# Performance work log

Measured on AMD Instinct MI355X. Metric: run time of the kernel, lower is better.

## Reference

```python
import jax, jax.numpy as jnp
import numpy as np

N = 50000      # nodes
E = 800000     # edges (avg degree 16)
IN = 128       # in_channels
OUT = 64       # out_channels (latent)
H = 2 * OUT    # hidden = 2*out_channels


def setup_inputs() -> dict:
    key = jax.random.key(0)
    ks = jax.random.split(key, 7)
    s = 0.1
    return {
        "x": jax.random.normal(ks[0], (N, IN), jnp.float32),
        "edge_index": jax.random.randint(ks[1], (2, E), 0, N, dtype=jnp.int64),
        "W1": jax.random.normal(ks[2], (IN, H), jnp.float32) * s,
        "b1": jnp.zeros((H,), jnp.float32),
        "Wmu": jax.random.normal(ks[3], (H, OUT), jnp.float32) * s,
        "bmu": jnp.zeros((OUT,), jnp.float32),
        "Wls": jax.random.normal(ks[4], (H, OUT), jnp.float32) * s,
        "bls": jnp.zeros((OUT,), jnp.float32),
        "eps": jax.random.normal(ks[5], (N, OUT), jnp.float32),
    }


def _gcn_conv(x, W, b, src, dst, dinv):
    # GCNConv: h = W x, out = D^-1/2 (A + I) D^-1/2 h + b
    h = x @ W                                   # [N, F]
    norm = (dinv[src] * dinv[dst])[:, None]     # [E, 1]
    agg = jax.ops.segment_sum(h[src] * norm, dst, num_segments=N)
    agg = agg + h * (dinv * dinv)[:, None]      # self-loop term
    return agg + b


def reference(x, edge_index, W1, b1, Wmu, bmu, Wls, bls, eps):
    src, dst = edge_index[0], edge_index[1]
    # degree with self-loops (PyG gcn_norm counts in-degree on dst/col)
    deg = jax.ops.segment_sum(jnp.ones((E,), x.dtype), dst, num_segments=N) + 1.0
    dinv = deg ** -0.5  # deg >= 1, safe

    h = jax.nn.relu(_gcn_conv(x, W1, b1, src, dst, dinv))
    mu = _gcn_conv(h, Wmu, bmu, src, dst, dinv)
    # Faithful to source bug: logstd also uses convmu weights
    logstd = _gcn_conv(h, Wmu, bmu, src, dst, dinv)
    # training-mode reparameterization with externally supplied noise
    zeta = mu + eps * jnp.exp(logstd)
    return (mu, logstd, zeta)
```

## Files before the change

### kernel.cpp

```cpp
#include <hip/hip_runtime.h>
#include <math.h>

#define N_NODES 50000
#define NPAD    50048
#define N_EDGES 800000
#define IN_C    128
#define H_C     128
#define OUT_C   64
#define BCAP    64
#define EPB     2048

typedef unsigned short u16;
typedef unsigned int   u32;

__device__ __forceinline__ u16 f2bf(float f) {
    u32 u; __builtin_memcpy(&u, &f, 4);
    u += 0x7FFFu + ((u >> 16) & 1u);
    return (u16)(u >> 16);
}
__device__ __forceinline__ float bflo(u32 p) { u32 u = p << 16;         float f; __builtin_memcpy(&f, &u, 4); return f; }
__device__ __forceinline__ float bfhi(u32 p) { u32 u = p & 0xFFFF0000u; float f; __builtin_memcpy(&f, &u, 4); return f; }

__global__ void k_detect_i64(const int* __restrict__ ei, int* __restrict__ flag) {
    int t = threadIdx.x;
    int nz = 0;
    for (int i = t; i < 256; i += 64)
        if (ei[2 * i + 1] != 0) nz = 1;
    unsigned long long b = __ballot(nz != 0);
    if (t == 0) *flag = (b == 0ULL) ? 1 : 0;
}

__device__ __forceinline__ int eidx(const int* __restrict__ ei, size_t pos, int mode) {
    return mode ? ei[pos << 1] : ei[pos];
}

__global__ void k_sort(const int* __restrict__ ei, const int* __restrict__ flag,
                       int* __restrict__ cursor, u16* __restrict__ sorted_src) {
    const int part  = blockIdx.x & 7;
    const int chunk = blockIdx.x >> 3;
    const int base  = chunk * EPB;
    const int m = *flag;
    for (int i = threadIdx.x; i < EPB; i += 256) {
        int e = base + i;
        if (e >= N_EDGES) break;
        int d = eidx(ei, (size_t)N_EDGES + e, m);
        if ((d & 7) != part) continue;
        int s = eidx(ei, (size_t)e, m);
        int c = atomicAdd(&cursor[d], 1);
        if (c < BCAP) sorted_src[((size_t)d << 6) + c] = (u16)s;
    }
}

__global__ void k_dinv(const int* __restrict__ cursor, float* __restrict__ dinv) {
    int i = blockIdx.x * blockDim.x + threadIdx.x;
    if (i < N_NODES) dinv[i] = rsqrtf((float)cursor[i] + 1.0f);
}

__launch_bounds__(256, 4)
__global__ void k_gemm1(const float* __restrict__ X, const float* __restrict__ W,
                        const float* __restrict__ dinv, u16* __restrict__ outq) {
    __shared__ __align__(16) char xs[32768];
    const int tid = threadIdx.x, wv = tid >> 6, lane = tid & 63;
    const int row0 = blockIdx.x * 64 + wv * 16;
    const size_t limit = (size_t)N_NODES * IN_C * 4 - 1024;
    const char* Xb = (const char*)X;

#pragma unroll
    for (int chk = 0; chk < 8; ++chk) {
        size_t off = (size_t)row0 * 512 + (size_t)chk * 1024;
        if (off > limit) off = limit;
        __builtin_amdgcn_global_load_lds(
            (const __attribute__((address_space(1))) void*)(Xb + off + (size_t)lane * 16),
            (__attribute__((address_space(3))) void*)(xs + wv * 8192 + chk * 1024 + lane * 16),
            16, 0, 0);
    }
    asm volatile("s_waitcnt vmcnt(0)" ::: "memory");
    __builtin_amdgcn_sched_barrier(0);

    const int c4 = (lane & 31) * 4;
    const int rs = lane >> 5;

    float4 acc[8];
#pragma unroll
    for (int r = 0; r < 8; ++r) acc[r] = make_float4(0.f, 0.f, 0.f, 0.f);

#pragma unroll 2
    for (int k4 = 0; k4 < IN_C / 4; ++k4) {
        float4 xv[8];
#pragma unroll
        for (int r = 0; r < 8; ++r)
            xv[r] = *reinterpret_cast<const float4*>(
                &xs[wv * 8192 + (rs + r * 2) * 512 + k4 * 16]);
        float4 w0 = *reinterpret_cast<const float4*>(W + (size_t)(4 * k4 + 0) * H_C + c4);
        float4 w1 = *reinterpret_cast<const float4*>(W + (size_t)(4 * k4 + 1) * H_C + c4);
        float4 w2 = *reinterpret_cast<const float4*>(W + (size_t)(4 * k4 + 2) * H_C + c4);
        float4 w3 = *reinterpret_cast<const float4*>(W + (size_t)(4 * k4 + 3) * H_C + c4);
#pragma unroll
        for (int r = 0; r < 8; ++r) {
            acc[r].x = fmaf(xv[r].x, w0.x, acc[r].x);
            acc[r].y = fmaf(xv[r].x, w0.y, acc[r].y);
            acc[r].z = fmaf(xv[r].x, w0.z, acc[r].z);
            acc[r].w = fmaf(xv[r].x, w0.w, acc[r].w);
            acc[r].x = fmaf(xv[r].y, w1.x, acc[r].x);
            acc[r].y = fmaf(xv[r].y, w1.y, acc[r].y);
            acc[r].z = fmaf(xv[r].y, w1.z, acc[r].z);
            acc[r].w = fmaf(xv[r].y, w1.w, acc[r].w);
            acc[r].x = fmaf(xv[r].z, w2.x, acc[r].x);
            acc[r].y = fmaf(xv[r].z, w2.y, acc[r].y);
            acc[r].z = fmaf(xv[r].z, w2.z, acc[r].z);
            acc[r].w = fmaf(xv[r].z, w2.w, acc[r].w);
            acc[r].x = fmaf(xv[r].w, w3.x, acc[r].x);
            acc[r].y = fmaf(xv[r].w, w3.y, acc[r].y);
            acc[r].z = fmaf(xv[r].w, w3.z, acc[r].z);
            acc[r].w = fmaf(xv[r].w, w3.w, acc[r].w);
        }
    }

#pragma unroll
    for (int r = 0; r < 8; ++r) {
        int row = row0 + rs + r * 2;
        if (row < N_NODES) {
            float di = dinv[row];
            ushort4 o;
            o.x = f2bf(acc[r].x * di);
            o.y = f2bf(acc[r].y * di);
            o.z = f2bf(acc[r].z * di);
            o.w = f2bf(acc[r].w * di);
            *reinterpret_cast<ushort4*>(
                outq + (size_t)(c4 >> 4) * (NPAD * 16) + (size_t)row * 16 + (c4 & 15)) = o;
        }
    }
}

__launch_bounds__(256, 4)
__global__ void k_gemm2(const u16* __restrict__ gbuf, const float* __restrict__ W,
                        u16* __restrict__ outp) {
    __shared__ __align__(16) char xs[32768];
    const int tid = threadIdx.x, wv = tid >> 6, lane = tid & 63;
    const int row0 = blockIdx.x * 128 + wv * 32;
    const char* Gb = (const char*)gbuf;

#pragma unroll
    for (int g = 0; g < 8; ++g) {
        size_t off = (size_t)g * (NPAD * 32) + (size_t)row0 * 32;
        __builtin_amdgcn_global_load_lds(
            (const __attribute__((address_space(1))) void*)(Gb + off + (size_t)lane * 16),
            (__attribute__((address_space(3))) void*)(xs + wv * 8192 + g * 1024 + lane * 16),
            16, 0, 0);
    }
    asm volatile("s_waitcnt vmcnt(0)" ::: "memory");
    __builtin_amdgcn_sched_barrier(0);

    const int c4 = (lane & 15) * 4;
    const int rs = lane >> 4;

    float4 acc[8];
#pragma unroll
    for (int r = 0; r < 8; ++r) acc[r] = make_float4(0.f, 0.f, 0.f, 0.f);

#pragma unroll 2
    for (int k4 = 0; k4 < IN_C / 4; ++k4) {
        float4 xv[8];
#pragma unroll
        for (int r = 0; r < 8; ++r) {
            int rl = rs + r * 4;
            uint2 u = *reinterpret_cast<const uint2*>(
                &xs[wv * 8192 + (k4 >> 2) * 1024 + rl * 32 + (k4 & 3) * 8]);
            xv[r].x = bflo(u.x); xv[r].y = bfhi(u.x);
            xv[r].z = bflo(u.y); xv[r].w = bfhi(u.y);
        }
        float4 w0 = *reinterpret_cast<const float4*>(W + (size_t)(4 * k4 + 0) * OUT_C + c4);
        float4 w1 = *reinterpret_cast<const float4*>(W + (size_t)(4 * k4 + 1) * OUT_C + c4);
        float4 w2 = *reinterpret_cast<const float4*>(W + (size_t)(4 * k4 + 2) * OUT_C + c4);
        float4 w3 = *reinterpret_cast<const float4*>(W + (size_t)(4 * k4 + 3) * OUT_C + c4);
#pragma unroll
        for (int r = 0; r < 8; ++r) {
            acc[r].x = fmaf(xv[r].x, w0.x, acc[r].x);
            acc[r].y = fmaf(xv[r].x, w0.y, acc[r].y);
            acc[r].z = fmaf(xv[r].x, w0.z, acc[r].z);
            acc[r].w = fmaf(xv[r].x, w0.w, acc[r].w);
            acc[r].x = fmaf(xv[r].y, w1.x, acc[r].x);
            acc[r].y = fmaf(xv[r].y, w1.y, acc[r].y);
            acc[r].z = fmaf(xv[r].y, w1.z, acc[r].z);
            acc[r].w = fmaf(xv[r].y, w1.w, acc[r].w);
            acc[r].x = fmaf(xv[r].z, w2.x, acc[r].x);
            acc[r].y = fmaf(xv[r].z, w2.y, acc[r].y);
            acc[r].z = fmaf(xv[r].z, w2.z, acc[r].z);
            acc[r].w = fmaf(xv[r].z, w2.w, acc[r].w);
            acc[r].x = fmaf(xv[r].w, w3.x, acc[r].x);
            acc[r].y = fmaf(xv[r].w, w3.y, acc[r].y);
            acc[r].z = fmaf(xv[r].w, w3.z, acc[r].z);
            acc[r].w = fmaf(xv[r].w, w3.w, acc[r].w);
        }
    }

#pragma unroll
    for (int r = 0; r < 8; ++r) {
        int row = row0 + rs + r * 4;
        if (row < N_NODES) {
            ushort4 o;
            o.x = f2bf(acc[r].x);
            o.y = f2bf(acc[r].y);
            o.z = f2bf(acc[r].z);
            o.w = f2bf(acc[r].w);
            *reinterpret_cast<ushort4*>(
                outp + (size_t)(c4 >> 4) * (NPAD * 16) + (size_t)row * 16 + (c4 & 15)) = o;
        }
    }
}

template <int NGRP, int MODE>
__global__ void k_agg(const u16* __restrict__ sorted_src,
                      const int* __restrict__ cursor,
                      const float* __restrict__ dinv,
                      const u16* __restrict__ rows,
                      const float* __restrict__ bias,
                      const float* __restrict__ eps,
                      void* __restrict__ outbuf) {
    const int part  = blockIdx.x & 7;
    const int g     = part % NGRP;
    const int sub   = part / NGRP;
    const int RANGE = N_NODES / (8 / NGRP);
    const int node0 = sub * RANGE + (blockIdx.x >> 3) * 32;
    const int nlim  = sub * RANGE + RANGE;

    const int wv = threadIdx.x >> 6, lane = threadIdx.x & 63;
    const int cl = lane >> 3, pr = lane & 7;
    const int n  = node0 + wv * 8 + cl;
    const bool act = (n < nlim);

    int c = act ? cursor[n] : 0;
    if (c > BCAP) c = BCAP;
    const float di = act ? dinv[n] : 0.f;

    const u32* rw = reinterpret_cast<const u32*>(rows) + (size_t)g * (NPAD * 8);
    const u16* bk = sorted_src + ((size_t)n << 6);

    float a0 = 0.f, a1 = 0.f, b0 = 0.f, b1 = 0.f;
    int j = 0;
    for (; j + 4 <= c; j += 4) {
        ushort4 s4 = *reinterpret_cast<const ushort4*>(bk + j);
        u32 p0 = rw[(size_t)s4.x * 8 + pr];
        u32 p1 = rw[(size_t)s4.y * 8 + pr];
        u32 p2 = rw[(size_t)s4.z * 8 + pr];
        u32 p3 = rw[(size_t)s4.w * 8 + pr];
        a0 += bflo(p0) + bflo(p2);  a1 += bfhi(p0) + bfhi(p2);
        b0 += bflo(p1) + bflo(p3);  b1 += bfhi(p1) + bfhi(p3);
    }
    for (; j < c; ++j) {
        u32 p0 = rw[(size_t)bk[j] * 8 + pr];
        a0 += bflo(p0); a1 += bfhi(p0);
    }
    u32 sn = rw[(size_t)n * 8 + pr];
    const int ch = g * 16 + 2 * pr;
    float s0 = a0 + b0 + bflo(sn);
    float s1 = a1 + b1 + bfhi(sn);

    if (MODE == 0) {
        float px = fmaf(di, s0, bias[ch]);
        float py = fmaf(di, s1, bias[ch + 1]);
        u32 o = (u32)f2bf(di * fmaxf(px, 0.f)) | ((u32)f2bf(di * fmaxf(py, 0.f)) << 16);
        if (act)
            ((u32*)outbuf)[(size_t)g * (NPAD * 8) + (size_t)n * 8 + pr] = o;
    } else if (act) {
        float m0 = fmaf(di, s0, bias[ch]);
        float m1 = fmaf(di, s1, bias[ch + 1]);
        const int NM = N_NODES * OUT_C;
        int i = n * 64 + ch;
        float2 e = *reinterpret_cast<const float2*>(eps + i);
        float z0 = fmaf(e.x, expf(m0), m0);
        float z1 = fmaf(e.y, expf(m1), m1);
        float* o = (float*)outbuf;
        *reinterpret_cast<float2*>(o + i)          = make_float2(m0, m1);
        *reinterpret_cast<float2*>(o + NM + i)     = make_float2(m0, m1);
        *reinterpret_cast<float2*>(o + 2 * NM + i) = make_float2(z0, z1);
    }
}

extern "C" void kernel_launch(void* const* d_in, const int* in_sizes, int n_in,
                              void* d_out, int out_size, void* d_ws, size_t ws_size,
                              hipStream_t stream) {
    const float* x   = (const float*)d_in[0];
    const int*   ei  = (const int*)d_in[1];
    const float* W1  = (const float*)d_in[2];
    const float* b1  = (const float*)d_in[3];
    const float* Wmu = (const float*)d_in[4];
    const float* bmu = (const float*)d_in[5];
    const float* eps = (const float*)d_in[8];
    float* out = (float*)d_out;

    char* p = (char*)d_ws;
    int*  flag   = (int*)p;                        p += 16;
    int*  cursor = (int*)p;                        p += ((size_t)N_NODES * 4 + 15) / 16 * 16;
    float* dinv  = (float*)p;                      p += ((size_t)N_NODES * 4 + 15) / 16 * 16;
    u16* sorted  = (u16*)p;                        p += ((size_t)N_NODES * BCAP * 2 + 15) / 16 * 16;
    u16* bufA    = (u16*)p;                        p += (size_t)8 * NPAD * 32;
    u16* bufG    = (u16*)p;
    u16* bufP    = bufA;

    hipMemsetAsync(cursor, 0, (size_t)N_NODES * sizeof(int), stream);
    k_detect_i64<<<1, 64, 0, stream>>>(ei, flag);
    k_sort<<<8 * ((N_EDGES + EPB - 1) / EPB), 256, 0, stream>>>(ei, flag, cursor, sorted);
    k_dinv<<<(N_NODES + 255) / 256, 256, 0, stream>>>(cursor, dinv);

    k_gemm1<<<(N_NODES + 63) / 64, 256, 0, stream>>>(x, W1, dinv, bufA);
    k_agg<8, 0><<<8 * ((N_NODES + 31) / 32), 256, 0, stream>>>(
        sorted, cursor, dinv, bufA, b1, nullptr, bufG);
    k_gemm2<<<(N_NODES + 127) / 128, 256, 0, stream>>>(bufG, Wmu, bufP);
    k_agg<4, 1><<<8 * ((N_NODES / 2 + 31) / 32), 256, 0, stream>>>(
        sorted, cursor, dinv, bufP, bmu, eps, out);
}
```

Baseline: 202.5 us.

## Widen feature groups to 32 channels and map one wave per node

```diff
diff --git a/kernel.cpp b/kernel.cpp
--- a/kernel.cpp
+++ b/kernel.cpp
@@ -71,7 +71,7 @@
         if (off > limit) off = limit;
         __builtin_amdgcn_global_load_lds(
             (const __attribute__((address_space(1))) void*)(Xb + off + (size_t)lane * 16),
-            (__attribute__((address_space(3))) void*)(xs + wv * 8192 + chk * 1024 + lane * 16),
+            (__attribute__((address_space(3))) void*)(xs + wv * 8192 + chk * 1024),
             16, 0, 0);
     }
     asm volatile("s_waitcnt vmcnt(0)" ::: "memory");
@@ -127,7 +127,7 @@
             o.z = f2bf(acc[r].z * di);
             o.w = f2bf(acc[r].w * di);
             *reinterpret_cast<ushort4*>(
-                outq + (size_t)(c4 >> 4) * (NPAD * 16) + (size_t)row * 16 + (c4 & 15)) = o;
+                outq + (size_t)(c4 >> 5) * (NPAD * 32) + (size_t)row * 32 + (c4 & 31)) = o;
         }
     }
 }
@@ -141,11 +141,12 @@
     const char* Gb = (const char*)gbuf;
 
 #pragma unroll
-    for (int g = 0; g < 8; ++g) {
-        size_t off = (size_t)g * (NPAD * 32) + (size_t)row0 * 32;
+    for (int chk = 0; chk < 8; ++chk) {
+        int g2 = chk >> 1, half = chk & 1;
+        size_t off = (size_t)g2 * (NPAD * 64) + (size_t)(row0 + half * 16) * 64;
         __builtin_amdgcn_global_load_lds(
             (const __attribute__((address_space(1))) void*)(Gb + off + (size_t)lane * 16),
-            (__attribute__((address_space(3))) void*)(xs + wv * 8192 + g * 1024 + lane * 16),
+            (__attribute__((address_space(3))) void*)(xs + wv * 8192 + chk * 1024),
             16, 0, 0);
     }
     asm volatile("s_waitcnt vmcnt(0)" ::: "memory");
@@ -165,7 +166,7 @@
         for (int r = 0; r < 8; ++r) {
             int rl = rs + r * 4;
             uint2 u = *reinterpret_cast<const uint2*>(
-                &xs[wv * 8192 + (k4 >> 2) * 1024 + rl * 32 + (k4 & 3) * 8]);
+                &xs[wv * 8192 + (k4 >> 3) * 2048 + rl * 64 + (k4 & 7) * 8]);
             xv[r].x = bflo(u.x); xv[r].y = bfhi(u.x);
             xv[r].z = bflo(u.y); xv[r].w = bfhi(u.y);
         }
@@ -204,7 +205,7 @@
             o.z = f2bf(acc[r].z);
             o.w = f2bf(acc[r].w);
             *reinterpret_cast<ushort4*>(
-                outp + (size_t)(c4 >> 4) * (NPAD * 16) + (size_t)row * 16 + (c4 & 15)) = o;
+                outp + (size_t)(c4 >> 5) * (NPAD * 32) + (size_t)row * 32 + (c4 & 31)) = o;
         }
     }
 }
@@ -217,63 +218,59 @@
                       const float* __restrict__ bias,
                       const float* __restrict__ eps,
                       void* __restrict__ outbuf) {
-    const int part  = blockIdx.x & 7;
-    const int g     = part % NGRP;
-    const int sub   = part / NGRP;
+    const int part = blockIdx.x & 7;
+    const int g    = part % NGRP;
+    const int sub  = part / NGRP;
     const int RANGE = N_NODES / (8 / NGRP);
-    const int node0 = sub * RANGE + (blockIdx.x >> 3) * 32;
-    const int nlim  = sub * RANGE + RANGE;
 
     const int wv = threadIdx.x >> 6, lane = threadIdx.x & 63;
-    const int cl = lane >> 3, pr = lane & 7;
-    const int n  = node0 + wv * 8 + cl;
-    const bool act = (n < nlim);
-
-    int c = act ? cursor[n] : 0;
-    if (c > BCAP) c = BCAP;
-    const float di = act ? dinv[n] : 0.f;
-
-    const u32* rw = reinterpret_cast<const u32*>(rows) + (size_t)g * (NPAD * 8);
+    const int e4 = lane >> 4, pr = lane & 15;
+    const int n  = sub * RANGE + (blockIdx.x >> 3) * 4 + wv;
+
+    int c = cursor[n]; if (c > BCAP) c = BCAP;
+    const float di = dinv[n];
+    const u32* rw = reinterpret_cast<const u32*>(rows) + (size_t)g * (NPAD * 16);
     const u16* bk = sorted_src + ((size_t)n << 6);
 
-    float a0 = 0.f, a1 = 0.f, b0 = 0.f, b1 = 0.f;
-    int j = 0;
-    for (; j + 4 <= c; j += 4) {
-        ushort4 s4 = *reinterpret_cast<const ushort4*>(bk + j);
-        u32 p0 = rw[(size_t)s4.x * 8 + pr];
-        u32 p1 = rw[(size_t)s4.y * 8 + pr];
-        u32 p2 = rw[(size_t)s4.z * 8 + pr];
-        u32 p3 = rw[(size_t)s4.w * 8 + pr];
-        a0 += bflo(p0) + bflo(p2);  a1 += bfhi(p0) + bfhi(p2);
-        b0 += bflo(p1) + bflo(p3);  b1 += bfhi(p1) + bfhi(p3);
-    }
-    for (; j < c; ++j) {
-        u32 p0 = rw[(size_t)bk[j] * 8 + pr];
-        a0 += bflo(p0); a1 += bfhi(p0);
-    }
-    u32 sn = rw[(size_t)n * 8 + pr];
-    const int ch = g * 16 + 2 * pr;
-    float s0 = a0 + b0 + bflo(sn);
-    float s1 = a1 + b1 + bfhi(sn);
+    float a0 = 0.f, a1 = 0.f;
+    const int iters = (c + 3) >> 2;
+    for (int j = 0; j < iters; ++j) {
+        int ep = (j << 2) + e4;
+        u16 id = bk[ep];
+        u32 p0 = rw[(size_t)id * 16 + pr];
+        bool v = ep < c;
+        a0 += v ? bflo(p0) : 0.f;
+        a1 += v ? bfhi(p0) : 0.f;
+    }
+    a0 += __shfl_xor(a0, 16); a0 += __shfl_xor(a0, 32);
+    a1 += __shfl_xor(a1, 16); a1 += __shfl_xor(a1, 32);
+
+    u32 sn = rw[(size_t)n * 16 + pr];
+    float s0 = a0 + bflo(sn);
+    float s1 = a1 + bfhi(sn);
+    const int ch = g * 32 + 2 * pr;
 
     if (MODE == 0) {
-        float px = fmaf(di, s0, bias[ch]);
-        float py = fmaf(di, s1, bias[ch + 1]);
-        u32 o = (u32)f2bf(di * fmaxf(px, 0.f)) | ((u32)f2bf(di * fmaxf(py, 0.f)) << 16);
-        if (act)
-            ((u32*)outbuf)[(size_t)g * (NPAD * 8) + (size_t)n * 8 + pr] = o;
-    } else if (act) {
-        float m0 = fmaf(di, s0, bias[ch]);
-        float m1 = fmaf(di, s1, bias[ch + 1]);
-        const int NM = N_NODES * OUT_C;
-        int i = n * 64 + ch;
-        float2 e = *reinterpret_cast<const float2*>(eps + i);
-        float z0 = fmaf(e.x, expf(m0), m0);
-        float z1 = fmaf(e.y, expf(m1), m1);
-        float* o = (float*)outbuf;
-        *reinterpret_cast<float2*>(o + i)          = make_float2(m0, m1);
-        *reinterpret_cast<float2*>(o + NM + i)     = make_float2(m0, m1);
-        *reinterpret_cast<float2*>(o + 2 * NM + i) = make_float2(z0, z1);
+        if (e4 == 0) {
+            float px = fmaf(di, s0, bias[ch]);
+            float py = fmaf(di, s1, bias[ch + 1]);
+            u32 o = (u32)f2bf(di * fmaxf(px, 0.f)) | ((u32)f2bf(di * fmaxf(py, 0.f)) << 16);
+            ((u32*)outbuf)[(size_t)g * (NPAD * 16) + (size_t)n * 16 + pr] = o;
+        }
+    } else {
+        if (e4 == 0) {
+            float m0 = fmaf(di, s0, bias[ch]);
+            float m1 = fmaf(di, s1, bias[ch + 1]);
+            const int NM = N_NODES * OUT_C;
+            int i = n * 64 + ch;
+            float2 e = *reinterpret_cast<const float2*>(eps + i);
+            float z0 = fmaf(e.x, expf(m0), m0);
+            float z1 = fmaf(e.y, expf(m1), m1);
+            float* o = (float*)outbuf;
+            *reinterpret_cast<float2*>(o + i)          = make_float2(m0, m1);
+            *reinterpret_cast<float2*>(o + NM + i)     = make_float2(m0, m1);
+            *reinterpret_cast<float2*>(o + 2 * NM + i) = make_float2(z0, z1);
+        }
     }
 }
 
@@ -294,7 +291,7 @@
     int*  cursor = (int*)p;                        p += ((size_t)N_NODES * 4 + 15) / 16 * 16;
     float* dinv  = (float*)p;                      p += ((size_t)N_NODES * 4 + 15) / 16 * 16;
     u16* sorted  = (u16*)p;                        p += ((size_t)N_NODES * BCAP * 2 + 15) / 16 * 16;
-    u16* bufA    = (u16*)p;                        p += (size_t)8 * NPAD * 32;
+    u16* bufA    = (u16*)p;                        p += (size_t)4 * NPAD * 64;
     u16* bufG    = (u16*)p;
     u16* bufP    = bufA;
 
@@ -304,9 +301,9 @@
     k_dinv<<<(N_NODES + 255) / 256, 256, 0, stream>>>(cursor, dinv);
 
     k_gemm1<<<(N_NODES + 63) / 64, 256, 0, stream>>>(x, W1, dinv, bufA);
-    k_agg<8, 0><<<8 * ((N_NODES + 31) / 32), 256, 0, stream>>>(
+    k_agg<4, 0><<<8 * (25000 / 4), 256, 0, stream>>>(
         sorted, cursor, dinv, bufA, b1, nullptr, bufG);
     k_gemm2<<<(N_NODES + 127) / 128, 256, 0, stream>>>(bufG, Wmu, bufP);
-    k_agg<4, 1><<<8 * ((N_NODES / 2 + 31) / 32), 256, 0, stream>>>(
+    k_agg<2, 1><<<8 * (12500 / 4), 256, 0, stream>>>(
         sorted, cursor, dinv, bufP, bmu, eps, out);
 }
```

Result: slower. 249.8 us (+23.4%).

## Widen feature groups to 32 channels, pad degree counters, retile GEMM1 and aggregation

Applied to the files above, without the earlier changes.

```diff
diff --git a/kernel.cpp b/kernel.cpp
--- a/kernel.cpp
+++ b/kernel.cpp
@@ -2,13 +2,13 @@
 #include <math.h>
 
 #define N_NODES 50000
-#define NPAD    50048
 #define N_EDGES 800000
 #define IN_C    128
 #define H_C     128
 #define OUT_C   64
 #define BCAP    64
 #define EPB     2048
+#define CSTRIDE 16
 
 typedef unsigned short u16;
 typedef unsigned int   u32;
@@ -46,32 +46,32 @@
         int d = eidx(ei, (size_t)N_EDGES + e, m);
         if ((d & 7) != part) continue;
         int s = eidx(ei, (size_t)e, m);
-        int c = atomicAdd(&cursor[d], 1);
+        int c = atomicAdd(&cursor[(size_t)d << 4], 1);
         if (c < BCAP) sorted_src[((size_t)d << 6) + c] = (u16)s;
     }
 }
 
 __global__ void k_dinv(const int* __restrict__ cursor, float* __restrict__ dinv) {
     int i = blockIdx.x * blockDim.x + threadIdx.x;
-    if (i < N_NODES) dinv[i] = rsqrtf((float)cursor[i] + 1.0f);
-}
-
-__launch_bounds__(256, 4)
+    if (i < N_NODES) dinv[i] = rsqrtf((float)cursor[(size_t)i << 4] + 1.0f);
+}
+
+__launch_bounds__(512, 6)
 __global__ void k_gemm1(const float* __restrict__ X, const float* __restrict__ W,
                         const float* __restrict__ dinv, u16* __restrict__ outq) {
     __shared__ __align__(16) char xs[32768];
     const int tid = threadIdx.x, wv = tid >> 6, lane = tid & 63;
-    const int row0 = blockIdx.x * 64 + wv * 16;
-    const size_t limit = (size_t)N_NODES * IN_C * 4 - 1024;
+    const int row0 = blockIdx.x * 64 + wv * 8;
+    const size_t limit = (size_t)N_NODES * 512 - 1024;
     const char* Xb = (const char*)X;
 
 #pragma unroll
-    for (int chk = 0; chk < 8; ++chk) {
+    for (int chk = 0; chk < 4; ++chk) {
         size_t off = (size_t)row0 * 512 + (size_t)chk * 1024;
         if (off > limit) off = limit;
         __builtin_amdgcn_global_load_lds(
             (const __attribute__((address_space(1))) void*)(Xb + off + (size_t)lane * 16),
-            (__attribute__((address_space(3))) void*)(xs + wv * 8192 + chk * 1024 + lane * 16),
+            (__attribute__((address_space(3))) void*)(xs + wv * 4096 + chk * 1024),
             16, 0, 0);
     }
     asm volatile("s_waitcnt vmcnt(0)" ::: "memory");
@@ -80,21 +80,104 @@
     const int c4 = (lane & 31) * 4;
     const int rs = lane >> 5;
 
-    float4 acc[8];
-#pragma unroll
-    for (int r = 0; r < 8; ++r) acc[r] = make_float4(0.f, 0.f, 0.f, 0.f);
+    float4 acc[4];
+#pragma unroll
+    for (int r = 0; r < 4; ++r) acc[r] = make_float4(0.f, 0.f, 0.f, 0.f);
 
 #pragma unroll 2
     for (int k4 = 0; k4 < IN_C / 4; ++k4) {
-        float4 xv[8];
-#pragma unroll
-        for (int r = 0; r < 8; ++r)
+        float4 xv[4];
+#pragma unroll
+        for (int r = 0; r < 4; ++r)
             xv[r] = *reinterpret_cast<const float4*>(
-                &xs[wv * 8192 + (rs + r * 2) * 512 + k4 * 16]);
+                &xs[wv * 4096 + (rs + r * 2) * 512 + k4 * 16]);
         float4 w0 = *reinterpret_cast<const float4*>(W + (size_t)(4 * k4 + 0) * H_C + c4);
         float4 w1 = *reinterpret_cast<const float4*>(W + (size_t)(4 * k4 + 1) * H_C + c4);
         float4 w2 = *reinterpret_cast<const float4*>(W + (size_t)(4 * k4 + 2) * H_C + c4);
         float4 w3 = *reinterpret_cast<const float4*>(W + (size_t)(4 * k4 + 3) * H_C + c4);
+#pragma unroll
+        for (int r = 0; r < 4; ++r) {
+            acc[r].x = fmaf(xv[r].x, w0.x, acc[r].x);
+            acc[r].y = fmaf(xv[r].x, w0.y, acc[r].y);
+            acc[r].z = fmaf(xv[r].x, w0.z, acc[r].z);
+            acc[r].w = fmaf(xv[r].x, w0.w, acc[r].w);
+            acc[r].x = fmaf(xv[r].y, w1.x, acc[r].x);
+            acc[r].y = fmaf(xv[r].y, w1.y, acc[r].y);
+            acc[r].z = fmaf(xv[r].y, w1.z, acc[r].z);
+            acc[r].w = fmaf(xv[r].y, w1.w, acc[r].w);
+            acc[r].x = fmaf(xv[r].z, w2.x, acc[r].x);
+            acc[r].y = fmaf(xv[r].z, w2.y, acc[r].y);
+            acc[r].z = fmaf(xv[r].z, w2.z, acc[r].z);
+            acc[r].w = fmaf(xv[r].z, w2.w, acc[r].w);
+            acc[r].x = fmaf(xv[r].w, w3.x, acc[r].x);
+            acc[r].y = fmaf(xv[r].w, w3.y, acc[r].y);
+            acc[r].z = fmaf(xv[r].w, w3.z, acc[r].z);
+            acc[r].w = fmaf(xv[r].w, w3.w, acc[r].w);
+        }
+    }
+
+#pragma unroll
+    for (int r = 0; r < 4; ++r) {
+        int row = row0 + rs + r * 2;
+        if (row < N_NODES) {
+            float di = dinv[row];
+            ushort4 o;
+            o.x = f2bf(acc[r].x * di);
+            o.y = f2bf(acc[r].y * di);
+            o.z = f2bf(acc[r].z * di);
+            o.w = f2bf(acc[r].w * di);
+            *reinterpret_cast<ushort4*>(
+                outq + (size_t)(c4 >> 5) * ((size_t)N_NODES * 32)
+                     + (size_t)row * 32 + (c4 & 31)) = o;
+        }
+    }
+}
+
+__launch_bounds__(256, 4)
+__global__ void k_gemm2(const u16* __restrict__ gbuf, const float* __restrict__ W,
+                        u16* __restrict__ outp) {
+    __shared__ __align__(16) char xs[32768];
+    const int tid = threadIdx.x, wv = tid >> 6, lane = tid & 63;
+    const int row0 = blockIdx.x * 128 + wv * 32;
+    const size_t gmax = (size_t)N_NODES * 64 - 1024;
+    const char* Gb = (const char*)gbuf;
+
+#pragma unroll
+    for (int chk = 0; chk < 8; ++chk) {
+        int grp = chk >> 1, half = chk & 1;
+        size_t goff = (size_t)(row0 + half * 16) * 64;
+        if (goff > gmax) goff = gmax;
+        size_t off = (size_t)grp * ((size_t)N_NODES * 64) + goff;
+        __builtin_amdgcn_global_load_lds(
+            (const __attribute__((address_space(1))) void*)(Gb + off + (size_t)lane * 16),
+            (__attribute__((address_space(3))) void*)(xs + wv * 8192 + grp * 2048 + half * 1024),
+            16, 0, 0);
+    }
+    asm volatile("s_waitcnt vmcnt(0)" ::: "memory");
+    __builtin_amdgcn_sched_barrier(0);
+
+    const int c4 = (lane & 15) * 4;
+    const int rs = lane >> 4;
+
+    float4 acc[8];
+#pragma unroll
+    for (int r = 0; r < 8; ++r) acc[r] = make_float4(0.f, 0.f, 0.f, 0.f);
+
+#pragma unroll 2
+    for (int k4 = 0; k4 < IN_C / 4; ++k4) {
+        float4 xv[8];
+#pragma unroll
+        for (int r = 0; r < 8; ++r) {
+            int rl = rs + r * 4;
+            uint2 u = *reinterpret_cast<const uint2*>(
+                &xs[wv * 8192 + (k4 >> 3) * 2048 + rl * 64 + (k4 & 7) * 8]);
+            xv[r].x = bflo(u.x); xv[r].y = bfhi(u.x);
+            xv[r].z = bflo(u.y); xv[r].w = bfhi(u.y);
+        }
+        float4 w0 = *reinterpret_cast<const float4*>(W + (size_t)(4 * k4 + 0) * OUT_C + c4);
+        float4 w1 = *reinterpret_cast<const float4*>(W + (size_t)(4 * k4 + 1) * OUT_C + c4);
+        float4 w2 = *reinterpret_cast<const float4*>(W + (size_t)(4 * k4 + 2) * OUT_C + c4);
+        float4 w3 = *reinterpret_cast<const float4*>(W + (size_t)(4 * k4 + 3) * OUT_C + c4);
 #pragma unroll
         for (int r = 0; r < 8; ++r) {
             acc[r].x = fmaf(xv[r].x, w0.x, acc[r].x);
@@ -118,84 +201,6 @@
 
 #pragma unroll
     for (int r = 0; r < 8; ++r) {
-        int row = row0 + rs + r * 2;
-        if (row < N_NODES) {
-            float di = dinv[row];
-            ushort4 o;
-            o.x = f2bf(acc[r].x * di);
-            o.y = f2bf(acc[r].y * di);
-            o.z = f2bf(acc[r].z * di);
-            o.w = f2bf(acc[r].w * di);
-            *reinterpret_cast<ushort4*>(
-                outq + (size_t)(c4 >> 4) * (NPAD * 16) + (size_t)row * 16 + (c4 & 15)) = o;
-        }
-    }
-}
-
-__launch_bounds__(256, 4)
-__global__ void k_gemm2(const u16* __restrict__ gbuf, const float* __restrict__ W,
-                        u16* __restrict__ outp) {
-    __shared__ __align__(16) char xs[32768];
-    const int tid = threadIdx.x, wv = tid >> 6, lane = tid & 63;
-    const int row0 = blockIdx.x * 128 + wv * 32;
-    const char* Gb = (const char*)gbuf;
-
-#pragma unroll
-    for (int g = 0; g < 8; ++g) {
-        size_t off = (size_t)g * (NPAD * 32) + (size_t)row0 * 32;
-        __builtin_amdgcn_global_load_lds(
-            (const __attribute__((address_space(1))) void*)(Gb + off + (size_t)lane * 16),
-            (__attribute__((address_space(3))) void*)(xs + wv * 8192 + g * 1024 + lane * 16),
-            16, 0, 0);
-    }
-    asm volatile("s_waitcnt vmcnt(0)" ::: "memory");
-    __builtin_amdgcn_sched_barrier(0);
-
-    const int c4 = (lane & 15) * 4;
-    const int rs = lane >> 4;
-
-    float4 acc[8];
-#pragma unroll
-    for (int r = 0; r < 8; ++r) acc[r] = make_float4(0.f, 0.f, 0.f, 0.f);
-
-#pragma unroll 2
-    for (int k4 = 0; k4 < IN_C / 4; ++k4) {
-        float4 xv[8];
-#pragma unroll
-        for (int r = 0; r < 8; ++r) {
-            int rl = rs + r * 4;
-            uint2 u = *reinterpret_cast<const uint2*>(
-                &xs[wv * 8192 + (k4 >> 2) * 1024 + rl * 32 + (k4 & 3) * 8]);
-            xv[r].x = bflo(u.x); xv[r].y = bfhi(u.x);
-            xv[r].z = bflo(u.y); xv[r].w = bfhi(u.y);
-        }
-        float4 w0 = *reinterpret_cast<const float4*>(W + (size_t)(4 * k4 + 0) * OUT_C + c4);
-        float4 w1 = *reinterpret_cast<const float4*>(W + (size_t)(4 * k4 + 1) * OUT_C + c4);
-        float4 w2 = *reinterpret_cast<const float4*>(W + (size_t)(4 * k4 + 2) * OUT_C + c4);
-        float4 w3 = *reinterpret_cast<const float4*>(W + (size_t)(4 * k4 + 3) * OUT_C + c4);
-#pragma unroll
-        for (int r = 0; r < 8; ++r) {
-            acc[r].x = fmaf(xv[r].x, w0.x, acc[r].x);
-            acc[r].y = fmaf(xv[r].x, w0.y, acc[r].y);
-            acc[r].z = fmaf(xv[r].x, w0.z, acc[r].z);
-            acc[r].w = fmaf(xv[r].x, w0.w, acc[r].w);
-            acc[r].x = fmaf(xv[r].y, w1.x, acc[r].x);
-            acc[r].y = fmaf(xv[r].y, w1.y, acc[r].y);
-            acc[r].z = fmaf(xv[r].y, w1.z, acc[r].z);
-            acc[r].w = fmaf(xv[r].y, w1.w, acc[r].w);
-            acc[r].x = fmaf(xv[r].z, w2.x, acc[r].x);
-            acc[r].y = fmaf(xv[r].z, w2.y, acc[r].y);
-            acc[r].z = fmaf(xv[r].z, w2.z, acc[r].z);
-            acc[r].w = fmaf(xv[r].z, w2.w, acc[r].w);
-            acc[r].x = fmaf(xv[r].w, w3.x, acc[r].x);
-            acc[r].y = fmaf(xv[r].w, w3.y, acc[r].y);
-            acc[r].z = fmaf(xv[r].w, w3.z, acc[r].z);
-            acc[r].w = fmaf(xv[r].w, w3.w, acc[r].w);
-        }
-    }
-
-#pragma unroll
-    for (int r = 0; r < 8; ++r) {
         int row = row0 + rs + r * 4;
         if (row < N_NODES) {
             ushort4 o;
@@ -204,7 +209,8 @@
             o.z = f2bf(acc[r].z);
             o.w = f2bf(acc[r].w);
             *reinterpret_cast<ushort4*>(
-                outp + (size_t)(c4 >> 4) * (NPAD * 16) + (size_t)row * 16 + (c4 & 15)) = o;
+                outp + (size_t)(c4 >> 5) * ((size_t)N_NODES * 32)
+                     + (size_t)row * 32 + (c4 & 31)) = o;
         }
     }
 }
@@ -217,51 +223,49 @@
                       const float* __restrict__ bias,
                       const float* __restrict__ eps,
                       void* __restrict__ outbuf) {
-    const int part  = blockIdx.x & 7;
-    const int g     = part % NGRP;
-    const int sub   = part / NGRP;
-    const int RANGE = N_NODES / (8 / NGRP);
-    const int node0 = sub * RANGE + (blockIdx.x >> 3) * 32;
-    const int nlim  = sub * RANGE + RANGE;
+    const int part = blockIdx.x & 7;
+    const int g    = part % NGRP;
+    const int sub  = part / NGRP;
+    const int RANGE = N_NODES * NGRP / 8;
 
     const int wv = threadIdx.x >> 6, lane = threadIdx.x & 63;
-    const int cl = lane >> 3, pr = lane & 7;
-    const int n  = node0 + wv * 8 + cl;
-    const bool act = (n < nlim);
-
-    int c = act ? cursor[n] : 0;
+    const int nd = lane >> 4, pr = lane & 15;
+    const int n  = sub * RANGE + (blockIdx.x >> 3) * 16 + wv * 4 + nd;
+    const bool act = (n < N_NODES);
+
+    int c = act ? cursor[(size_t)n << 4] : 0;
     if (c > BCAP) c = BCAP;
     const float di = act ? dinv[n] : 0.f;
-
-    const u32* rw = reinterpret_cast<const u32*>(rows) + (size_t)g * (NPAD * 8);
-    const u16* bk = sorted_src + ((size_t)n << 6);
+    const u32* rw = reinterpret_cast<const u32*>(rows) + (size_t)g * ((size_t)N_NODES * 16);
+    const u16* bk = sorted_src + ((size_t)(act ? n : 0) << 6);
+    u32 sn = act ? rw[(size_t)n * 16 + pr] : 0;
 
     float a0 = 0.f, a1 = 0.f, b0 = 0.f, b1 = 0.f;
     int j = 0;
     for (; j + 4 <= c; j += 4) {
         ushort4 s4 = *reinterpret_cast<const ushort4*>(bk + j);
-        u32 p0 = rw[(size_t)s4.x * 8 + pr];
-        u32 p1 = rw[(size_t)s4.y * 8 + pr];
-        u32 p2 = rw[(size_t)s4.z * 8 + pr];
-        u32 p3 = rw[(size_t)s4.w * 8 + pr];
+        u32 p0 = rw[(size_t)s4.x * 16 + pr];
+        u32 p1 = rw[(size_t)s4.y * 16 + pr];
+        u32 p2 = rw[(size_t)s4.z * 16 + pr];
+        u32 p3 = rw[(size_t)s4.w * 16 + pr];
         a0 += bflo(p0) + bflo(p2);  a1 += bfhi(p0) + bfhi(p2);
         b0 += bflo(p1) + bflo(p3);  b1 += bfhi(p1) + bfhi(p3);
     }
     for (; j < c; ++j) {
-        u32 p0 = rw[(size_t)bk[j] * 8 + pr];
+        u32 p0 = rw[(size_t)bk[j] * 16 + pr];
         a0 += bflo(p0); a1 += bfhi(p0);
     }
-    u32 sn = rw[(size_t)n * 8 + pr];
-    const int ch = g * 16 + 2 * pr;
-    float s0 = a0 + b0 + bflo(sn);
-    float s1 = a1 + b1 + bfhi(sn);
+    float s0 = (a0 + b0) + bflo(sn);
+    float s1 = (a1 + b1) + bfhi(sn);
+    const int ch = g * 32 + 2 * pr;
 
     if (MODE == 0) {
-        float px = fmaf(di, s0, bias[ch]);
-        float py = fmaf(di, s1, bias[ch + 1]);
-        u32 o = (u32)f2bf(di * fmaxf(px, 0.f)) | ((u32)f2bf(di * fmaxf(py, 0.f)) << 16);
-        if (act)
-            ((u32*)outbuf)[(size_t)g * (NPAD * 8) + (size_t)n * 8 + pr] = o;
+        if (act) {
+            float px = fmaf(di, s0, bias[ch]);
+            float py = fmaf(di, s1, bias[ch + 1]);
+            u32 o = (u32)f2bf(di * fmaxf(px, 0.f)) | ((u32)f2bf(di * fmaxf(py, 0.f)) << 16);
+            ((u32*)outbuf)[(size_t)g * ((size_t)N_NODES * 16) + (size_t)n * 16 + pr] = o;
+        }
     } else if (act) {
         float m0 = fmaf(di, s0, bias[ch]);
         float m1 = fmaf(di, s1, bias[ch + 1]);
@@ -291,22 +295,22 @@
 
     char* p = (char*)d_ws;
     int*  flag   = (int*)p;                        p += 16;
-    int*  cursor = (int*)p;                        p += ((size_t)N_NODES * 4 + 15) / 16 * 16;
+    int*  cursor = (int*)p;                        p += (size_t)N_NODES * CSTRIDE * 4;
     float* dinv  = (float*)p;                      p += ((size_t)N_NODES * 4 + 15) / 16 * 16;
     u16* sorted  = (u16*)p;                        p += ((size_t)N_NODES * BCAP * 2 + 15) / 16 * 16;
-    u16* bufA    = (u16*)p;                        p += (size_t)8 * NPAD * 32;
+    u16* bufA    = (u16*)p;                        p += ((size_t)N_NODES * H_C * 2 + 15) / 16 * 16;
     u16* bufG    = (u16*)p;
     u16* bufP    = bufA;
 
-    hipMemsetAsync(cursor, 0, (size_t)N_NODES * sizeof(int), stream);
+    hipMemsetAsync(cursor, 0, (size_t)N_NODES * CSTRIDE * sizeof(int), stream);
     k_detect_i64<<<1, 64, 0, stream>>>(ei, flag);
     k_sort<<<8 * ((N_EDGES + EPB - 1) / EPB), 256, 0, stream>>>(ei, flag, cursor, sorted);
     k_dinv<<<(N_NODES + 255) / 256, 256, 0, stream>>>(cursor, dinv);
 
-    k_gemm1<<<(N_NODES + 63) / 64, 256, 0, stream>>>(x, W1, dinv, bufA);
-    k_agg<8, 0><<<8 * ((N_NODES + 31) / 32), 256, 0, stream>>>(
+    k_gemm1<<<(N_NODES + 63) / 64, 512, 0, stream>>>(x, W1, dinv, bufA);
+    k_agg<4, 0><<<8 * ((25000 + 15) / 16), 256, 0, stream>>>(
         sorted, cursor, dinv, bufA, b1, nullptr, bufG);
     k_gemm2<<<(N_NODES + 127) / 128, 256, 0, stream>>>(bufG, Wmu, bufP);
-    k_agg<4, 1><<<8 * ((N_NODES / 2 + 31) / 32), 256, 0, stream>>>(
+    k_agg<2, 1><<<8 * ((12500 + 15) / 16), 256, 0, stream>>>(
         sorted, cursor, dinv, bufP, bmu, eps, out);
 }
```

Measured after the change: 188.8 us. -6.8%, faster.
